# Optimization experiments

Measured on AMD Instinct MI355X. Metric: run time of the kernel, lower is better.

The kernel has to match this reference:

```python
import jax, jax.numpy as jnp
import numpy as np

B, S, D = 32, 64, 16
OUT_F = 8
IN_DIM = S * D                      # 1024
N_QUAD = (IN_DIM + IN_DIM ** 2) // 2  # 524800 upper-triangular (incl. diag) entries
OUT_DIM = OUT_F * S                 # 512

# Static upper-triangular indices (row-major, includes diagonal) — same order as
# torch.triu_indices(in_dim, in_dim).
_TRIU_R, _TRIU_C = np.triu_indices(IN_DIM)


def setup_inputs() -> dict:
    key = jax.random.key(0)
    k1, k2, k3 = jax.random.split(key, 3)
    input_ = jax.random.normal(k1, (B, S, D), dtype=jnp.float32)
    in_total = IN_DIM + N_QUAD
    bound = 1.0 / np.sqrt(in_total)
    W = jax.random.uniform(k2, (OUT_DIM, in_total), dtype=jnp.float32, minval=-bound, maxval=bound)
    b = jax.random.uniform(k3, (OUT_DIM,), dtype=jnp.float32, minval=-bound, maxval=bound)
    return {"input_": input_, "W": W, "b": b}


def reference(input_, W, b):
    Bsz = input_.shape[0]
    x_flat = input_.reshape(Bsz, IN_DIM)                     # [B, in_dim]
    r = jnp.asarray(_TRIU_R)
    c = jnp.asarray(_TRIU_C)
    # Quadratic features: upper-triangular entries of outer(x, x) without
    # materializing the full [B, in_dim, in_dim] outer product.
    x_squared = x_flat[:, r] * x_flat[:, c]                  # [B, N_QUAD]
    x = jnp.concatenate([x_flat, x_squared], axis=-1)        # [B, in_dim + N_QUAD]
    out = x @ W.T + b                                        # [B, out_f * S]
    return out.reshape(Bsz, S, OUT_F)
```

## Files before the change

### kernel.cpp

```cpp
#include <hip/hip_runtime.h>
#include <hip/hip_bf16.h>

#define B_SZ     32
#define IN_DIM   1024
#define K_TOTAL  525824
#define OUT_DIM  512
#define NCH      4108
#define KGN      128
#define P_BYTES  ((size_t)KGN * B_SZ * OUT_DIM * 4)
#define XT_BYTES ((size_t)IN_DIM * B_SZ * 4)
#define NEED_WS  (P_BYTES + XT_BYTES)

typedef __attribute__((ext_vector_type(8))) short bfrag;
typedef __attribute__((ext_vector_type(4))) float f32x4;

#define GLD16(g, l) __builtin_amdgcn_global_load_lds(                      \
    (const __attribute__((address_space(1))) void*)(g),                    \
    (__attribute__((address_space(3))) void*)(l), 16, 0, 0)

__device__ inline unsigned bf16r(float f)
{
    unsigned u = __builtin_bit_cast(unsigned, f);
    return (u + 0x7FFFu + ((u >> 16) & 1u)) >> 16;
}
__device__ inline unsigned pk2(float a, float b)
{
    return bf16r(a) | (bf16r(b) << 16);
}

__global__ void bias_init_kernel(const float* __restrict__ bias, float* __restrict__ out)
{
    int i = blockIdx.x * 256 + threadIdx.x;
    out[i] = bias[i & (OUT_DIM - 1)];
}

__global__ __launch_bounds__(256)
void xpose_kernel(const float* __restrict__ x, float* __restrict__ xT)
{
    const int idx = blockIdx.x * 256 + threadIdx.x;
    const int k = idx >> 5, b = idx & 31;
    xT[idx] = x[b * IN_DIM + k];
}

__global__ __launch_bounds__(256, 2)
void qgemm_mfma_kernel(const float* __restrict__ xT,
                       const float* __restrict__ W,
                       float* __restrict__ partial)
{
    __shared__ int4 wlds[2][64][32];
    __shared__ int4 fbuf[2][512];

    const int tid  = threadIdx.x;
    const int lane = tid & 63;
    const int wv_  = tid >> 6;
    const int lrow = lane & 15;
    const int lkb  = lane >> 4;

    const int og = blockIdx.x >> 7;
    const int kg = blockIdx.x & (KGN - 1);

    const int o_blk  = og * 64;
    const int o_base = o_blk + wv_ * 16;

    f32x4 acc0 = {0.f, 0.f, 0.f, 0.f};
    f32x4 acc1 = {0.f, 0.f, 0.f, 0.f};

    #define WSTAGE(s, cc)                                                       \
    do {                                                                        \
        _Pragma("unroll")                                                       \
        for (int j_ = 0; j_ < 8; ++j_) {                                        \
            const int rl_ = 2 * j_ + (lane >> 5);                               \
            const char* src_ = (const char*)(W                                  \
                + (size_t)(o_blk + wv_ * 16 + rl_) * K_TOTAL                    \
                + (size_t)(cc) * 128)                                           \
                + (((lane & 31) << 4) ^ ((rl_ & 7) << 4));                      \
            GLD16(src_, (char*)&wlds[s][wv_ * 16 + 2 * j_][0]);                 \
        }                                                                       \
    } while (0)

    #define FCOMP(s, cc)                                                        \
    do {                                                                        \
        _Pragma("unroll")                                                       \
        for (int i_ = 0; i_ < 2; ++i_) {                                        \
            const int u_  = tid + i_ * 256;           \
            const int kb_ = u_ >> 5;                                            \
            const int b_  = u_ & 31;                                            \
            const int k0_ = (cc) * 128 + kb_ * 8;                               \
            float v_[8];                                                        \
            if (k0_ < IN_DIM) {                                                 \
                _Pragma("unroll")                                               \
                for (int e_ = 0; e_ < 8; ++e_)                                  \
                    v_[e_] = xT[(k0_ + e_) * B_SZ + b_];                        \
            } else {                                                            \
                int t_ = k0_ - IN_DIM;                                          \
                float disc_ = 4198401.0f - 8.0f * (float)t_;                    \
                int r_ = (int)((2049.0f - sqrtf(disc_)) * 0.5f);                \
                int off_ = r_ * IN_DIM - ((r_ * (r_ - 1)) >> 1);                \
                if (t_ < off_) { --r_; off_ = r_ * IN_DIM - ((r_ * (r_ - 1)) >> 1); } \
                else if (t_ >= off_ + (IN_DIM - r_)) { off_ += IN_DIM - r_; ++r_; }   \
                int c2_ = r_ + (t_ - off_);                                     \
                _Pragma("unroll")                                               \
                for (int e_ = 0; e_ < 8; ++e_) {                                \
                    v_[e_] = xT[r_ * B_SZ + b_] * xT[c2_ * B_SZ + b_];          \
                    if (c2_ == IN_DIM - 1) { ++r_; c2_ = r_; } else { ++c2_; }  \
                }                                                               \
            }                                                                   \
            int4 pk_;                                                           \
            pk_.x = (int)pk2(v_[0], v_[1]);                                     \
            pk_.y = (int)pk2(v_[2], v_[3]);                                     \
            pk_.z = (int)pk2(v_[4], v_[5]);                                     \
            pk_.w = (int)pk2(v_[6], v_[7]);                                     \
            fbuf[s][u_] = pk_;                                                  \
        }                                                                       \
    } while (0)

    #define COMPUTE(s)                                                          \
    do {                                                                        \
        const int r_  = wv_ * 16 + lrow;                                        \
        const int s7_ = lrow & 7;                                               \
        _Pragma("unroll")                                                       \
        for (int q_ = 0; q_ < 4; ++q_) {                                        \
            const int sl_ = lkb * 2 + q_ * 8;                                   \
            const float4 f0_ = __builtin_bit_cast(float4, wlds[s][r_][sl_ ^ s7_]);       \
            const float4 f1_ = __builtin_bit_cast(float4, wlds[s][r_][(sl_ + 1) ^ s7_]); \
            int4 tw_;                                                           \
            tw_.x = (int)pk2(f0_.x, f0_.y);                                     \
            tw_.y = (int)pk2(f0_.z, f0_.w);                                     \
            tw_.z = (int)pk2(f1_.x, f1_.y);                                     \
            tw_.w = (int)pk2(f1_.z, f1_.w);                                     \
            const bfrag bw_ = __builtin_bit_cast(bfrag, tw_);                   \
            const int ub_ = (q_ * 4 + lkb) * 32 + lrow;                         \
            const bfrag a0_ = __builtin_bit_cast(bfrag, fbuf[s][ub_]);          \
            const bfrag a1_ = __builtin_bit_cast(bfrag, fbuf[s][ub_ + 16]);     \
            acc0 = __builtin_amdgcn_mfma_f32_16x16x32_bf16(a0_, bw_, acc0, 0, 0, 0); \
            acc1 = __builtin_amdgcn_mfma_f32_16x16x32_bf16(a1_, bw_, acc1, 0, 0, 0); \
        }                                                                       \
    } while (0)

    const int n = (kg < 12) ? 33 : 32;
    int c = kg;

    FCOMP(0, c);
    FCOMP(1, c + KGN);
    __builtin_amdgcn_sched_barrier(0);
    WSTAGE(0, c);
    WSTAGE(1, c + KGN);

    for (int t = 0; t < n; ++t) {
        if (t < n - 1)
            asm volatile("s_waitcnt vmcnt(8) lgkmcnt(0)" ::: "memory");
        else
            asm volatile("s_waitcnt vmcnt(0) lgkmcnt(0)" ::: "memory");
        __builtin_amdgcn_s_barrier();
        COMPUTE(t & 1);
        __builtin_amdgcn_s_barrier();
        if (t + 2 < n) {
            FCOMP(t & 1, c + 2 * KGN);
            __builtin_amdgcn_sched_barrier(0);
            WSTAGE(t & 1, c + 2 * KGN);
        }
        c += KGN;
    }

    #undef COMPUTE
    #undef FCOMP
    #undef WSTAGE

    float* pb = partial + (size_t)kg * (B_SZ * OUT_DIM) + o_base + lrow;
    const int r0 = lkb * 4;
    #pragma unroll
    for (int r = 0; r < 4; ++r) {
        pb[(size_t)(r0 + r) * OUT_DIM]      = acc0[r];
        pb[(size_t)(16 + r0 + r) * OUT_DIM] = acc1[r];
    }
}

__global__ __launch_bounds__(256)
void reduce_kernel(const float* __restrict__ partial,
                   const float* __restrict__ bias,
                   float* __restrict__ out)
{
    const int idx = blockIdx.x * 256 + threadIdx.x;
    float s = bias[idx & (OUT_DIM - 1)];
    const float* p = partial + idx;
    #pragma unroll 8
    for (int kg = 0; kg < KGN; ++kg)
        s += p[(size_t)kg * (B_SZ * OUT_DIM)];
    out[idx] = s;
}

__global__ __launch_bounds__(512, 2)
void qgemm_fallback_kernel(const float* __restrict__ x,
                           const float* __restrict__ W,
                           float* __restrict__ out)
{
    __shared__ float xt[B_SZ][512];

    const int tid  = threadIdx.x;
    const int lane = tid & 63;
    const int wave = tid >> 6;
    const int bgrp = wave & 3;
    const int ogrp = wave >> 2;

    const int og  = blockIdx.x & 31;
    const int kgf = blockIdx.x >> 5;

    const int o_base = og * 16 + ogrp * 8;
    const int b_base = bgrp * 8;

    float acc[8][8];
    #pragma unroll
    for (int i = 0; i < 8; ++i)
        #pragma unroll
        for (int o = 0; o < 8; ++o) acc[i][o] = 0.f;

    const int nch = (K_TOTAL + 511) / 512;
    for (int chunk = kgf; chunk < nch; chunk += 16) {
        const int k = chunk * 512 + tid;
        __syncthreads();
        if (k < IN_DIM) {
            #pragma unroll
            for (int b = 0; b < B_SZ; ++b)
                xt[b][tid] = x[b * IN_DIM + k];
        } else {
            const int t = k - IN_DIM;
            double disc = 4198401.0 - 8.0 * (double)t;
            int r = (int)((2049.0 - sqrt(disc)) * 0.5);
            int off = r * IN_DIM - ((r * (r - 1)) >> 1);
            if (t < off) { --r; off = r * IN_DIM - ((r * (r - 1)) >> 1); }
            else if (t >= off + (IN_DIM - r)) { off += IN_DIM - r; ++r; }
            const int ccol = r + (t - off);
            #pragma unroll
            for (int b = 0; b < B_SZ; ++b)
                xt[b][tid] = x[b * IN_DIM + r] * x[b * IN_DIM + ccol];
        }
        __syncthreads();

        const float* wrow = W + (size_t)o_base * K_TOTAL + (size_t)chunk * 512;
        #pragma unroll
        for (int pass = 0; pass < 2; ++pass) {
            const int kk = pass * 256 + lane * 4;
            float4 wv[8];
            #pragma unroll
            for (int o = 0; o < 8; ++o)
                wv[o] = *(const float4*)(wrow + (size_t)o * K_TOTAL + kk);
            float4 xv[8];
            #pragma unroll
            for (int i = 0; i < 8; ++i)
                xv[i] = *(const float4*)&xt[b_base + i][kk];
            #pragma unroll
            for (int o = 0; o < 8; ++o)
                #pragma unroll
                for (int i = 0; i < 8; ++i)
                    acc[i][o] += xv[i].x * wv[o].x + xv[i].y * wv[o].y
                               + xv[i].z * wv[o].z + xv[i].w * wv[o].w;
        }
    }

    #pragma unroll
    for (int i = 0; i < 8; ++i)
        #pragma unroll
        for (int o = 0; o < 8; ++o) {
            float v = acc[i][o];
            #pragma unroll
            for (int m = 1; m < 64; m <<= 1)
                v += __shfl_xor(v, m);
            acc[i][o] = v;
        }

    if (lane == 0) {
        #pragma unroll
        for (int i = 0; i < 8; ++i)
            #pragma unroll
            for (int o = 0; o < 8; ++o)
                atomicAdd(&out[(b_base + i) * OUT_DIM + o_base + o], acc[i][o]);
    }
}

extern "C" void kernel_launch(void* const* d_in, const int* in_sizes, int n_in,
                              void* d_out, int out_size, void* d_ws, size_t ws_size,
                              hipStream_t stream)
{
    const float* x    = (const float*)d_in[0];
    const float* W    = (const float*)d_in[1];
    const float* bias = (const float*)d_in[2];
    float* out = (float*)d_out;

    if (ws_size >= NEED_WS) {
        float* part = (float*)d_ws;
        float* xT   = (float*)((char*)d_ws + P_BYTES);
        hipLaunchKernelGGL(xpose_kernel, dim3(128), dim3(256), 0, stream, x, xT);
        hipLaunchKernelGGL(qgemm_mfma_kernel, dim3(8 * KGN), dim3(256), 0, stream,
                           xT, W, part);
        hipLaunchKernelGGL(reduce_kernel, dim3(64), dim3(256), 0, stream,
                           part, bias, out);
    } else {
        hipLaunchKernelGGL(bias_init_kernel, dim3(64), dim3(256), 0, stream, bias, out);
        hipLaunchKernelGGL(qgemm_fallback_kernel, dim3(512), dim3(512), 0, stream,
                           x, W, out);
    }
}
```

Before: 258.5 us.

## Make each wave independent with private LDS buffers and drop block barriers

After: 540.7 us. 2.09x slower.

```diff
diff --git a/kernel.cpp b/kernel.cpp
--- a/kernel.cpp
+++ b/kernel.cpp
@@ -5,9 +5,9 @@
 #define IN_DIM   1024
 #define K_TOTAL  525824
 #define OUT_DIM  512
-#define NCH      4108
-#define KGN      128
-#define P_BYTES  ((size_t)KGN * B_SZ * OUT_DIM * 4)
+#define NCH64    8216
+#define KSEG     64
+#define P_BYTES  ((size_t)KSEG * B_SZ * OUT_DIM * 4)
 #define XT_BYTES ((size_t)IN_DIM * B_SZ * 4)
 #define NEED_WS  (P_BYTES + XT_BYTES)
 
@@ -47,8 +47,8 @@
                        const float* __restrict__ W,
                        float* __restrict__ partial)
 {
-    __shared__ int4 wlds[2][64][32];
-    __shared__ int4 fbuf[2][512];
+    __shared__ int4 wbuf[4][2][16][16];
+    __shared__ int4 fbuf[4][2][256];
 
     const int tid  = threadIdx.x;
     const int lane = tid & 63;
@@ -56,11 +56,11 @@
     const int lrow = lane & 15;
     const int lkb  = lane >> 4;
 
-    const int og = blockIdx.x >> 7;
-    const int kg = blockIdx.x & (KGN - 1);
-
-    const int o_blk  = og * 64;
-    const int o_base = o_blk + wv_ * 16;
+    const int gw   = blockIdx.x * 4 + wv_;
+    const int og   = gw >> 6;
+    const int kseg = gw & 63;
+
+    const int o_base = og * 16;
 
     f32x4 acc0 = {0.f, 0.f, 0.f, 0.f};
     f32x4 acc1 = {0.f, 0.f, 0.f, 0.f};
@@ -68,24 +68,23 @@
     #define WSTAGE(s, cc)                                                       \
     do {                                                                        \
         _Pragma("unroll")                                                       \
-        for (int j_ = 0; j_ < 8; ++j_) {                                        \
-            const int rl_ = 2 * j_ + (lane >> 5);                               \
+        for (int j_ = 0; j_ < 4; ++j_) {                                        \
+            const int row_ = 4 * j_ + (lane >> 4);                              \
             const char* src_ = (const char*)(W                                  \
-                + (size_t)(o_blk + wv_ * 16 + rl_) * K_TOTAL                    \
-                + (size_t)(cc) * 128)                                           \
-                + (((lane & 31) << 4) ^ ((rl_ & 7) << 4));                      \
-            GLD16(src_, (char*)&wlds[s][wv_ * 16 + 2 * j_][0]);                 \
+                + (size_t)(o_base + row_) * K_TOTAL + (size_t)(cc) * 64)        \
+                + ((((lane & 15) << 4)) ^ ((row_ & 7) << 4));                   \
+            GLD16(src_, (char*)&wbuf[wv_][s][4 * j_][0]);                       \
         }                                                                       \
     } while (0)
 
     #define FCOMP(s, cc)                                                        \
     do {                                                                        \
         _Pragma("unroll")                                                       \
-        for (int i_ = 0; i_ < 2; ++i_) {                                        \
-            const int u_  = tid + i_ * 256;           \
-            const int kb_ = u_ >> 5;                                            \
+        for (int i_ = 0; i_ < 4; ++i_) {                                        \
+            const int u_  = lane + i_ * 64;           \
+            const int kb_ = u_ >> 5;                                  \
             const int b_  = u_ & 31;                                            \
-            const int k0_ = (cc) * 128 + kb_ * 8;                               \
+            const int k0_ = (cc) * 64 + kb_ * 8;                                \
             float v_[8];                                                        \
             if (k0_ < IN_DIM) {                                                 \
                 _Pragma("unroll")                                               \
@@ -110,19 +109,18 @@
             pk_.y = (int)pk2(v_[2], v_[3]);                                     \
             pk_.z = (int)pk2(v_[4], v_[5]);                                     \
             pk_.w = (int)pk2(v_[6], v_[7]);                                     \
-            fbuf[s][u_] = pk_;                                                  \
+            fbuf[wv_][s][u_] = pk_;                                             \
         }                                                                       \
     } while (0)
 
     #define COMPUTE(s)                                                          \
     do {                                                                        \
-        const int r_  = wv_ * 16 + lrow;                                        \
         const int s7_ = lrow & 7;                                               \
         _Pragma("unroll")                                                       \
-        for (int q_ = 0; q_ < 4; ++q_) {                                        \
-            const int sl_ = lkb * 2 + q_ * 8;                                   \
-            const float4 f0_ = __builtin_bit_cast(float4, wlds[s][r_][sl_ ^ s7_]);       \
-            const float4 f1_ = __builtin_bit_cast(float4, wlds[s][r_][(sl_ + 1) ^ s7_]); \
+        for (int q_ = 0; q_ < 2; ++q_) {                                        \
+            const int sl_ = q_ * 8 + lkb * 2;                                   \
+            const float4 f0_ = __builtin_bit_cast(float4, wbuf[wv_][s][lrow][sl_ ^ s7_]);       \
+            const float4 f1_ = __builtin_bit_cast(float4, wbuf[wv_][s][lrow][(sl_ + 1) ^ s7_]); \
             int4 tw_;                                                           \
             tw_.x = (int)pk2(f0_.x, f0_.y);                                     \
             tw_.y = (int)pk2(f0_.z, f0_.w);                                     \
@@ -130,43 +128,41 @@
             tw_.w = (int)pk2(f1_.z, f1_.w);                                     \
             const bfrag bw_ = __builtin_bit_cast(bfrag, tw_);                   \
             const int ub_ = (q_ * 4 + lkb) * 32 + lrow;                         \
-            const bfrag a0_ = __builtin_bit_cast(bfrag, fbuf[s][ub_]);          \
-            const bfrag a1_ = __builtin_bit_cast(bfrag, fbuf[s][ub_ + 16]);     \
+            const bfrag a0_ = __builtin_bit_cast(bfrag, fbuf[wv_][s][ub_]);     \
+            const bfrag a1_ = __builtin_bit_cast(bfrag, fbuf[wv_][s][ub_ + 16]);\
             acc0 = __builtin_amdgcn_mfma_f32_16x16x32_bf16(a0_, bw_, acc0, 0, 0, 0); \
             acc1 = __builtin_amdgcn_mfma_f32_16x16x32_bf16(a1_, bw_, acc1, 0, 0, 0); \
         }                                                                       \
     } while (0)
 
-    const int n = (kg < 12) ? 33 : 32;
-    int c = kg;
+    const int n = (kseg < 24) ? 129 : 128;
+    int c = kseg;
 
     FCOMP(0, c);
-    FCOMP(1, c + KGN);
+    FCOMP(1, c + KSEG);
     __builtin_amdgcn_sched_barrier(0);
     WSTAGE(0, c);
-    WSTAGE(1, c + KGN);
+    WSTAGE(1, c + KSEG);
 
     for (int t = 0; t < n; ++t) {
         if (t < n - 1)
-            asm volatile("s_waitcnt vmcnt(8) lgkmcnt(0)" ::: "memory");
+            asm volatile("s_waitcnt vmcnt(4)" ::: "memory");
         else
-            asm volatile("s_waitcnt vmcnt(0) lgkmcnt(0)" ::: "memory");
-        __builtin_amdgcn_s_barrier();
+            asm volatile("s_waitcnt vmcnt(0)" ::: "memory");
         COMPUTE(t & 1);
-        __builtin_amdgcn_s_barrier();
         if (t + 2 < n) {
-            FCOMP(t & 1, c + 2 * KGN);
+            FCOMP(t & 1, c + 2 * KSEG);
             __builtin_amdgcn_sched_barrier(0);
-            WSTAGE(t & 1, c + 2 * KGN);
-        }
-        c += KGN;
+            WSTAGE(t & 1, c + 2 * KSEG);
+        }
+        c += KSEG;
     }
 
     #undef COMPUTE
     #undef FCOMP
     #undef WSTAGE
 
-    float* pb = partial + (size_t)kg * (B_SZ * OUT_DIM) + o_base + lrow;
+    float* pb = partial + (size_t)kseg * (B_SZ * OUT_DIM) + o_base + lrow;
     const int r0 = lkb * 4;
     #pragma unroll
     for (int r = 0; r < 4; ++r) {
@@ -184,7 +180,7 @@
     float s = bias[idx & (OUT_DIM - 1)];
     const float* p = partial + idx;
     #pragma unroll 8
-    for (int kg = 0; kg < KGN; ++kg)
+    for (int kg = 0; kg < KSEG; ++kg)
         s += p[(size_t)kg * (B_SZ * OUT_DIM)];
     out[idx] = s;
 }
@@ -290,7 +286,7 @@
         float* part = (float*)d_ws;
         float* xT   = (float*)((char*)d_ws + P_BYTES);
         hipLaunchKernelGGL(xpose_kernel, dim3(128), dim3(256), 0, stream, x, xT);
-        hipLaunchKernelGGL(qgemm_mfma_kernel, dim3(8 * KGN), dim3(256), 0, stream,
+        hipLaunchKernelGGL(qgemm_mfma_kernel, dim3(512), dim3(256), 0, stream,
                            xT, W, part);
         hipLaunchKernelGGL(reduce_kernel, dim3(64), dim3(256), 0, stream,
                            part, bias, out);
```
